# Performance work log

Measured on AMD Instinct MI355X. Metric: run time of the kernel, lower is better.

The kernel has to match this reference:

```python
import jax, jax.numpy as jnp
import numpy as np

EPS = 1e-5   # BatchNorm eps (eval mode, running_mean=0, running_var=1 as at init)
NEG = 0.2    # LeakyReLU negative slope


def _conv(W, x):
    # 1x1 conv == channel matmul. W: [out_c, in_c], x: [B, in_c, ...]
    return jnp.einsum('oc,bc...->bo...', W, x)


def _bn(x, g, b):
    # eval-mode BN with running_mean=0, running_var=1
    sh = (1, -1) + (1,) * (x.ndim - 2)
    return x * (g.reshape(sh) / np.float32(np.sqrt(1.0 + EPS))) + b.reshape(sh)


def _lrelu(x):
    return jax.nn.leaky_relu(x, NEG)


def _knn_idx(pos, k):
    # pos: [B, 3, N] -> idx [B, N, k] of k nearest points (incl. self)
    sq = jnp.sum(pos * pos, axis=1)                      # [B, N]
    inner = jnp.einsum('bcn,bcm->bnm', pos, pos)         # [B, N, N]
    dist = sq[:, :, None] + sq[:, None, :] - 2.0 * inner
    _, idx = jax.lax.top_k(-dist, k)
    return idx


def _gather(points, idx):
    # points [B, N, C], idx [B, N, K] -> [B, N, K, C]
    return jax.vmap(lambda p, i: p[i])(points, idx)


def setup_inputs() -> dict:
    key = jax.random.key(0)
    B, N, K = 2, 8192, 16
    d_points, d_model = 64, 64
    ks = jax.random.split(key, 24)
    w = lambda k_, o, i: (jax.random.normal(k_, (o, i), jnp.float32) * 0.05)
    gm = lambda k_, c: (1.0 + 0.1 * jax.random.normal(k_, (c,), jnp.float32))
    bt = lambda k_, c: (0.1 * jax.random.normal(k_, (c,), jnp.float32))
    return {
        'feats': jax.random.normal(ks[0], (B, d_points, N), jnp.float32),
        'pos': jax.random.uniform(ks[1], (B, 3, N), jnp.float32),
        'k': K,
        'W1': w(ks[2], d_model, d_points), 'g1': gm(ks[3], d_model), 'b1': bt(ks[4], d_model),
        'Wq': w(ks[5], d_model, d_model), 'Wk': w(ks[6], d_model, d_model), 'Wv': w(ks[7], d_model, d_model),
        'Wd1': w(ks[8], d_model, 3), 'gd1': gm(ks[9], d_model), 'bd1': bt(ks[10], d_model),
        'Wd2': w(ks[11], d_model, d_model), 'gd2': gm(ks[12], d_model), 'bd2': bt(ks[13], d_model),
        'Wg1': w(ks[14], d_model, d_model), 'gg1': gm(ks[15], d_model), 'bg1': bt(ks[16], d_model),
        'Wg2': w(ks[17], d_model, d_model), 'gg2': gm(ks[18], d_model), 'bg2': bt(ks[19], d_model),
        'W2': w(ks[20], d_points, d_model), 'g2': gm(ks[21], d_points), 'b2': bt(ks[22], d_points),
    }


def reference(feats, pos, k, W1, g1, b1, Wq, Wk, Wv,
              Wd1, gd1, bd1, Wd2, gd2, bd2,
              Wg1, gg1, bg1, Wg2, gg2, bg2, W2, g2, b2):
    B, _, N = feats.shape
    knn_idx = _knn_idx(pos, k)                            # [B, N, K]
    pos_nc = jnp.transpose(pos, (0, 2, 1))                # [B, N, 3]
    knn_pos = _gather(pos_nc, knn_idx)                    # [B, N, K, 3]

    x = _lrelu(_bn(_conv(W1, feats), g1, b1))             # [B, d, N]
    q = _conv(Wq, x)                                      # [B, d, N]
    k_feat = _gather(jnp.transpose(_conv(Wk, x), (0, 2, 1)), knn_idx)
    k_t = jnp.transpose(k_feat, (0, 3, 2, 1))             # [B, d, K, N]
    v_feat = _gather(jnp.transpose(_conv(Wv, x), (0, 2, 1)), knn_idx)
    v_t = jnp.transpose(v_feat, (0, 3, 2, 1))             # [B, d, K, N]

    rel = pos_nc[:, :, None, :] - knn_pos                 # [B, N, K, 3]
    rel_t = jnp.transpose(rel, (0, 3, 2, 1))              # [B, 3, K, N]
    pe = _lrelu(_bn(_conv(Wd1, rel_t), gd1, bd1))
    pos_enc = _lrelu(_bn(_conv(Wd2, pe), gd2, bd2))       # [B, d, K, N]

    a = q[:, :, None, :] - k_t + pos_enc                  # [B, d, K, N]
    a = _lrelu(_bn(_conv(Wg1, a), gg1, bg1))
    a = _lrelu(_bn(_conv(Wg2, a), gg2, bg2))
    # torch: attn / sqrt(k.size(-1)) where k has shape [B, d, K, N] -> sqrt(N)
    attn = jax.nn.softmax(a / jnp.sqrt(jnp.float32(N)), axis=-2)

    res = jnp.einsum('bmnf,bmnf->bmf', attn, v_t + pos_enc)  # [B, d, N]
    out = _lrelu(_bn(_conv(W2, res), g2, b2)) + feats
    return out
```

## Files before the change

### kernel.cpp

```cpp
#include <hip/hip_runtime.h>
#include <hip/hip_bf16.h>
#include <math.h>

namespace {

constexpr int B = 2;
constexpr int N = 8192;
constexpr int D = 64;
constexpr int GRID = 10;
constexpr int GC = GRID * GRID * GRID;
constexpr float H = 0.1f;
constexpr float NEGS = 0.2f;
constexpr float BN_INV = 0.9999950000374997f;
constexpr float RSQN = 0.011048543456039806f;

typedef __attribute__((ext_vector_type(8))) short bf16x8;
typedef __attribute__((ext_vector_type(16))) float f32x16;

union Frag { int4 i4; unsigned u[4]; bf16x8 h; };

__device__ __forceinline__ float lrelu(float v) { return v > 0.f ? v : NEGS * v; }

__device__ __forceinline__ unsigned pk2(float a, float b) {
  __hip_bfloat162 h2 = __float22bfloat162_rn(make_float2(a, b));
  unsigned r;
  __builtin_memcpy(&r, &h2, 4);
  return r;
}
__device__ __forceinline__ float blo(unsigned u) { return __uint_as_float(u << 16); }
__device__ __forceinline__ float bhi(unsigned u) { return __uint_as_float(u & 0xFFFF0000u); }

__device__ __forceinline__ f32x16 MF(int4 a, const Frag& b, f32x16 c) {
  Frag af; af.i4 = a;
  return __builtin_amdgcn_mfma_f32_32x32x16_bf16(af.h, b.h, c, 0, 0, 0);
}

__device__ __forceinline__ int cellco(float v) {
  int c = (int)(v * 10.0f);
  return min(max(c, 0), GRID - 1);
}

__device__ __forceinline__ void buildB(const f32x16& x0, const f32x16& x1, int h, Frag Bf[4]) {
  unsigned Z[8][2];
  #pragma unroll
  for (int q = 0; q < 4; ++q) {
    Z[q][0]     = pk2(x0[4*q+0], x0[4*q+1]);
    Z[q][1]     = pk2(x0[4*q+2], x0[4*q+3]);
    Z[4+q][0]   = pk2(x1[4*q+0], x1[4*q+1]);
    Z[4+q][1]   = pk2(x1[4*q+2], x1[4*q+3]);
  }
  unsigned S[8][2];
  #pragma unroll
  for (int q = 0; q < 8; ++q) {
    S[q][0] = (unsigned)__shfl_xor((int)Z[q][0], 32);
    S[q][1] = (unsigned)__shfl_xor((int)Z[q][1], 32);
  }
  #pragma unroll
  for (int t = 0; t < 4; ++t) {
    int qq = (t >> 1) * 4 + 2 * (t & 1);
    Bf[t].u[0] = h ? S[qq+1][0] : Z[qq][0];
    Bf[t].u[1] = h ? S[qq+1][1] : Z[qq][1];
    Bf[t].u[2] = h ? Z[qq+1][0] : S[qq][0];
    Bf[t].u[3] = h ? Z[qq+1][1] : S[qq][1];
  }
}

__device__ __forceinline__ f32x16 biasAct(f32x16 d, const float4* bp, int mt, int h) {
  f32x16 r;
  #pragma unroll
  for (int q = 0; q < 4; ++q) {
    float4 bb = bp[h * 8 + mt * 4 + q];
    r[4*q+0] = lrelu(d[4*q+0] + bb.x);
    r[4*q+1] = lrelu(d[4*q+1] + bb.y);
    r[4*q+2] = lrelu(d[4*q+2] + bb.z);
    r[4*q+3] = lrelu(d[4*q+3] + bb.w);
  }
  return r;
}

struct PrepArgs {
  const float* W[9];
  const float* scale[9];
  const float* bias[5];
  const float* bd1;
};

__global__ __launch_bounds__(256) void prep_kernel(PrepArgs a, unsigned short* AF, float* biasAll) {
  int mi = blockIdx.x;
  int tid = threadIdx.x;
  if (mi < 8) {
    int off = (mi == 7) ? 29696 : mi * 4096;
    const float* W = a.W[mi];
    const float* G = a.scale[mi];
    unsigned short* dst = AF + off;
    for (int e = tid; e < 4096; e += 256) {
      int i = e & 7, lane = (e >> 3) & 63, t = (e >> 9) & 3, mt = e >> 11;
      int row = 32 * mt + (lane & 31);
      int k = 16 * t + 8 * (lane >> 5) + i;
      float v = W[row * 64 + k];
      if (G) v *= G[row] * BN_INV;
      __hip_bfloat16 hb = __float2bfloat16(v);
      __builtin_memcpy(&dst[e], &hb, 2);
    }
  } else {
    const float* W = a.W[8];
    const float* G = a.scale[8];
    for (int e = tid; e < 1024; e += 256) {
      int i = e & 7, lane = (e >> 3) & 63, mt = e >> 9;
      int row = 32 * mt + (lane & 31), h = lane >> 5;
      float v = 0.f;
      if (h == 0) {
        if (i < 3) v = W[row * 3 + i] * G[row] * BN_INV;
        else if (i == 3) v = a.bd1[row];
      }
      __hip_bfloat16 hb = __float2bfloat16(v);
      __builtin_memcpy(&AF[28672 + e], &hb, 2);
    }
    for (int e = tid; e < 320; e += 256) {
      int ai = e >> 6, idx = e & 63;
      int h = idx >> 5, mt = (idx >> 4) & 1, q = (idx >> 2) & 3, j = idx & 3;
      biasAll[e] = a.bias[ai][32 * mt + 8 * q + 4 * h + j];
    }
  }
}

__global__ __launch_bounds__(256) void pos4cid_kernel(
    const float* __restrict__ pos, float* __restrict__ pos4,
    int* __restrict__ cid16, int* __restrict__ cellCount)
{
  int i = blockIdx.x * 256 + threadIdx.x;
  int b = i >> 13;
  int n = i & (N - 1);
  const float* pb = pos + (size_t)b * 3 * N;
  float x = pb[n], y = pb[N + n], z = pb[2 * N + n];
  float4 v = {x, y, z, x * x + y * y + z * z};
  *reinterpret_cast<float4*>(pos4 + (size_t)i * 4) = v;
  int cid = (cellco(z) * GRID + cellco(y)) * GRID + cellco(x);
  cid16[i] = cid;
  atomicAdd(&cellCount[b * GC + cid], 1);
}

__global__ __launch_bounds__(1024) void scan_kernel(
    const int* __restrict__ cnt, int* __restrict__ cellStart)
{
  __shared__ int s[2][2048];
  int t = threadIdx.x;
  s[0][t] = cnt[t];
  s[0][t + 1024] = cnt[t + 1024];
  __syncthreads();
  int src = 0;
  for (int off = 1; off < 2048; off <<= 1) {
    int dst = src ^ 1;
    for (int i = t; i < 2048; i += 1024) {
      int v = s[src][i];
      if (i >= off) v += s[src][i - off];
      s[dst][i] = v;
    }
    __syncthreads();
    src ^= 1;
  }
  cellStart[t] = (t == 0) ? 0 : s[src][t - 1];
  cellStart[t + 1024] = s[src][t + 1023];
}

__global__ __launch_bounds__(256) void scatter_kernel(
    const float* __restrict__ pos4, const int* __restrict__ cid16,
    const int* __restrict__ cellStart, int* __restrict__ cellOfs,
    float4* __restrict__ pos4s, int* __restrict__ sid)
{
  int i = blockIdx.x * 256 + threadIdx.x;
  int b = i >> 13;
  int cg = b * GC + cid16[i];
  int dst = cellStart[cg] + atomicAdd(&cellOfs[cg], 1);
  pos4s[dst] = *reinterpret_cast<const float4*>(pos4 + (size_t)i * 4);
  sid[dst] = i & (N - 1);
}

__global__ __launch_bounds__(256) void knn_shell_kernel(
    const float4* __restrict__ pos4s, const int* __restrict__ sid,
    const int* __restrict__ cellStart, int* __restrict__ knn)
{
  constexpr unsigned long long SENT = 0x7F7FFFFFFFFFFFFFULL;
  int lq = threadIdx.x & 15;
  int wid = (blockIdx.x * 256 + threadIdx.x) >> 4;
  int b = wid >> 13;
  float4 q = pos4s[wid];
  int myid = sid[wid];
  int cx = cellco(q.x), cy = cellco(q.y), cz = cellco(q.z);
  const int cbase = b * GC;
  int* orow = knn + ((size_t)b * N + myid) * 16;

  bool done = false;
  #pragma unroll 1
  for (int r = 1; r < GRID; ++r) {
    if (!done) {
      unsigned long long dk[16];
      #pragma unroll
      for (int j = 0; j < 16; ++j) dk[j] = SENT;

      int x0 = max(cx - r, 0), x1 = min(cx + r, GRID - 1);
      int y0 = max(cy - r, 0), y1 = min(cy + r, GRID - 1);
      int z0 = max(cz - r, 0), z1 = min(cz + r, GRID - 1);
      #pragma unroll 1
      for (int zz = z0; zz <= z1; ++zz) {
        #pragma unroll 1
        for (int yy = y0; yy <= y1; ++yy) {
          int rowc = cbase + (zz * GRID + yy) * GRID;
          int i0 = cellStart[rowc + x0], i1 = cellStart[rowc + x1 + 1];
          #pragma unroll 1
          for (int i = i0 + lq; i < i1; i += 16) {
            float4 cp = pos4s[i];
            float inn = q.x * cp.x + q.y * cp.y + q.z * cp.z;
            float dist = fmaxf(fmaf(-2.f, inn, q.w + cp.w), 0.f);
            unsigned long long key =
                ((unsigned long long)__float_as_uint(dist) << 32) | (unsigned)sid[i];
            if (key < dk[15]) {
              bool bj = true;
              #pragma unroll
              for (int j = 15; j >= 1; --j) {
                bool bjm1 = key < dk[j - 1];
                dk[j] = bj ? (bjm1 ? dk[j - 1] : key) : dk[j];
                bj = bjm1;
              }
              if (bj) dk[0] = key;
            }
          }
        }
      }

      float dlast = 0.f;
      #pragma unroll 1
      for (int e = 0; e < 16; ++e) {
        unsigned long long m = dk[0];
        #pragma unroll
        for (int msk = 1; msk <= 8; msk <<= 1) {
          unsigned long long o = __shfl_xor(m, msk);
          m = (o < m) ? o : m;
        }
        if (dk[0] == m) {
          #pragma unroll
          for (int j = 0; j < 15; ++j) dk[j] = dk[j + 1];
          dk[15] = SENT;
        }
        if (lq == 0) orow[e] = (int)(m & 0xFFFFFFFFULL);
        dlast = __uint_as_float((unsigned)(m >> 32));
      }

      float mg = 3.4e38f;
      if (cx - r > 0)        mg = fminf(mg, q.x - (cx - r) * H);
      if (cx + r < GRID - 1) mg = fminf(mg, (cx + r + 1) * H - q.x);
      if (cy - r > 0)        mg = fminf(mg, q.y - (cy - r) * H);
      if (cy + r < GRID - 1) mg = fminf(mg, (cy + r + 1) * H - q.y);
      if (cz - r > 0)        mg = fminf(mg, q.z - (cz - r) * H);
      if (cz + r < GRID - 1) mg = fminf(mg, (cz + r + 1) * H - q.z);
      done = (dlast <= mg * mg * 0.999f);
    }
    if (__all(done)) break;
  }
}

__global__ __launch_bounds__(256) void qkv_kernel(
    const float* __restrict__ feats, const int4* __restrict__ AF,
    const float* __restrict__ b1p,
    uint2* __restrict__ qT, uint2* __restrict__ kT, uint2* __restrict__ vT)
{
  __shared__ int4 sA[2048];
  for (int i = threadIdx.x; i < 2048; i += 256) sA[i] = AF[i];
  __syncthreads();
  int lane = threadIdx.x & 63, w = threadIdx.x >> 6;
  int gw = blockIdx.x * 4 + w;
  int col = lane & 31, h = lane >> 5;
  int nb = gw * 32;
  int b = nb >> 13;
  int n = (nb & (N - 1)) + col;
  size_t gpt = (size_t)b * N + n;
  const float* fb = feats + (size_t)b * D * N + n;

  Frag Bf[4];
  #pragma unroll
  for (int t = 0; t < 4; ++t) {
    int c0 = 16 * t + 8 * h;
    float f[8];
    #pragma unroll
    for (int i = 0; i < 8; ++i) f[i] = fb[(size_t)(c0 + i) * N];
    #pragma unroll
    for (int d_ = 0; d_ < 4; ++d_) Bf[t].u[d_] = pk2(f[2*d_], f[2*d_+1]);
  }
  f32x16 acc0 = {}, acc1 = {};
  #pragma unroll
  for (int t = 0; t < 4; ++t) {
    acc0 = MF(sA[t * 64 + lane], Bf[t], acc0);
    acc1 = MF(sA[(4 + t) * 64 + lane], Bf[t], acc1);
  }
  const float4* bp = (const float4*)b1p;
  f32x16 x0 = biasAct(acc0, bp, 0, h);
  f32x16 x1 = biasAct(acc1, bp, 1, h);
  Frag Bx[4];
  buildB(x0, x1, h, Bx);

  #pragma unroll
  for (int mmat = 0; mmat < 3; ++mmat) {
    const int4* Am = sA + 512 * (mmat + 1);
    uint2* op = (mmat == 0) ? qT : (mmat == 1) ? kT : vT;
    f32x16 a0 = {}, a1 = {};
    #pragma unroll
    for (int t = 0; t < 4; ++t) {
      a0 = MF(Am[t * 64 + lane], Bx[t], a0);
      a1 = MF(Am[(4 + t) * 64 + lane], Bx[t], a1);
    }
    #pragma unroll
    for (int q = 0; q < 4; ++q) {
      uint2 v0, v1;
      v0.x = pk2(a0[4*q+0], a0[4*q+1]); v0.y = pk2(a0[4*q+2], a0[4*q+3]);
      v1.x = pk2(a1[4*q+0], a1[4*q+1]); v1.y = pk2(a1[4*q+2], a1[4*q+3]);
      op[gpt * 16 + 2 * q + h] = v0;
      op[gpt * 16 + 8 + 2 * q + h] = v1;
    }
  }
}

__global__ __launch_bounds__(256) void fused_kernel(
    const float4* __restrict__ pos4, const int* __restrict__ knn,
    const uint2* __restrict__ qT, const uint2* __restrict__ kT, const uint2* __restrict__ vT,
    const int4* __restrict__ AF,
    const float* __restrict__ biases,
    float* __restrict__ res_ws)
{
  __shared__ int4 sA[1664];
  for (int i = threadIdx.x; i < 1664; i += 256) sA[i] = AF[i];
  __syncthreads();
  const float4* bpd2 = (const float4*)(biases);
  const float4* bpg1 = (const float4*)(biases + 64);
  const float4* bpg2 = (const float4*)(biases + 128);

  int lane = threadIdx.x & 63, w = threadIdx.x >> 6;
  int gw = blockIdx.x * 4 + w;
  int col = lane & 31, h = lane >> 5;
  int p = col >> 4, kk = col & 15;
  int pbase = gw * 2;
  int b = pbase >> 13;
  int n = (pbase & (N - 1)) + p;
  size_t g = (size_t)b * N + n;
  int m = knn[g * 16 + kk];
  size_t gm = (size_t)b * N + m;

  float4 P = pos4[g], Q = pos4[gm];
  float rx = P.x - Q.x, ry = P.y - Q.y, rz = P.z - Q.z;

  Frag B0;
  B0.u[0] = h ? 0u : pk2(rx, ry);
  B0.u[1] = h ? 0u : pk2(rz, 1.0f);
  B0.u[2] = 0u; B0.u[3] = 0u;
  f32x16 acc0 = {}, acc1 = {};
  acc0 = MF(sA[1536 + lane], B0, acc0);
  acc1 = MF(sA[1536 + 64 + lane], B0, acc1);
  f32x16 pe0, pe1;
  #pragma unroll
  for (int i = 0; i < 16; ++i) { pe0[i] = lrelu(acc0[i]); pe1[i] = lrelu(acc1[i]); }
  Frag Bp[4];
  buildB(pe0, pe1, h, Bp);

  acc0 = (f32x16){}; acc1 = (f32x16){};
  #pragma unroll
  for (int t = 0; t < 4; ++t) {
    acc0 = MF(sA[t * 64 + lane], Bp[t], acc0);
    acc1 = MF(sA[(4 + t) * 64 + lane], Bp[t], acc1);
  }
  f32x16 pn0 = biasAct(acc0, bpd2, 0, h);
  f32x16 pn1 = biasAct(acc1, bpd2, 1, h);

  unsigned pep[8][2];
  #pragma unroll
  for (int q = 0; q < 4; ++q) {
    pep[q][0]   = pk2(pn0[4*q+0], pn0[4*q+1]);
    pep[q][1]   = pk2(pn0[4*q+2], pn0[4*q+3]);
    pep[4+q][0] = pk2(pn1[4*q+0], pn1[4*q+1]);
    pep[4+q][1] = pk2(pn1[4*q+2], pn1[4*q+3]);
  }

  f32x16 av0, av1;
  #pragma unroll
  for (int mt = 0; mt < 2; ++mt) {
    f32x16& dst = mt ? av1 : av0;
    const f32x16& pn = mt ? pn1 : pn0;
    #pragma unroll
    for (int q = 0; q < 4; ++q) {
      uint2 qv = qT[g * 16 + 8 * mt + 2 * q + h];
      uint2 kv = kT[gm * 16 + 8 * mt + 2 * q + h];
      dst[4*q+0] = pn[4*q+0] + blo(qv.x) - blo(kv.x);
      dst[4*q+1] = pn[4*q+1] + bhi(qv.x) - bhi(kv.x);
      dst[4*q+2] = pn[4*q+2] + blo(qv.y) - blo(kv.y);
      dst[4*q+3] = pn[4*q+3] + bhi(qv.y) - bhi(kv.y);
    }
  }
  buildB(av0, av1, h, Bp);

  acc0 = (f32x16){}; acc1 = (f32x16){};
  #pragma unroll
  for (int t = 0; t < 4; ++t) {
    acc0 = MF(sA[512 + t * 64 + lane], Bp[t], acc0);
    acc1 = MF(sA[512 + (4 + t) * 64 + lane], Bp[t], acc1);
  }
  f32x16 a10 = biasAct(acc0, bpg1, 0, h);
  f32x16 a11 = biasAct(acc1, bpg1, 1, h);
  buildB(a10, a11, h, Bp);

  acc0 = (f32x16){}; acc1 = (f32x16){};
  #pragma unroll
  for (int t = 0; t < 4; ++t) {
    acc0 = MF(sA[1024 + t * 64 + lane], Bp[t], acc0);
    acc1 = MF(sA[1024 + (4 + t) * 64 + lane], Bp[t], acc1);
  }
  f32x16 at0 = biasAct(acc0, bpg2, 0, h);
  f32x16 at1 = biasAct(acc1, bpg2, 1, h);
  #pragma unroll
  for (int i = 0; i < 16; ++i) { at0[i] *= RSQN; at1[i] *= RSQN; }

  float* rp = res_ws + g * 64;
  #pragma unroll
  for (int mt = 0; mt < 2; ++mt) {
    const f32x16& at = mt ? at1 : at0;
    f32x16 ev, nm;
    #pragma unroll
    for (int q = 0; q < 4; ++q) {
      uint2 vv = vT[gm * 16 + 8 * mt + 2 * q + h];
      unsigned pp0 = pep[mt * 4 + q][0], pp1 = pep[mt * 4 + q][1];
      float vp0 = blo(vv.x) + blo(pp0);
      float vp1 = bhi(vv.x) + bhi(pp0);
      float vp2 = blo(vv.y) + blo(pp1);
      float vp3 = bhi(vv.y) + bhi(pp1);
      ev[4*q+0] = __expf(at[4*q+0]); nm[4*q+0] = ev[4*q+0] * vp0;
      ev[4*q+1] = __expf(at[4*q+1]); nm[4*q+1] = ev[4*q+1] * vp1;
      ev[4*q+2] = __expf(at[4*q+2]); nm[4*q+2] = ev[4*q+2] * vp2;
      ev[4*q+3] = __expf(at[4*q+3]); nm[4*q+3] = ev[4*q+3] * vp3;
    }
    #pragma unroll
    for (int i = 0; i < 16; ++i) {
      #pragma unroll
      for (int mask = 1; mask <= 8; mask <<= 1) {
        ev[i] += __shfl_xor(ev[i], mask);
        nm[i] += __shfl_xor(nm[i], mask);
      }
    }
    if (kk == 0) {
      #pragma unroll
      for (int q = 0; q < 4; ++q) {
        float4 r;
        r.x = nm[4*q+0] / ev[4*q+0];
        r.y = nm[4*q+1] / ev[4*q+1];
        r.z = nm[4*q+2] / ev[4*q+2];
        r.w = nm[4*q+3] / ev[4*q+3];
        *(float4*)(rp + 32 * mt + 8 * q + 4 * h) = r;
      }
    }
  }
}

__global__ __launch_bounds__(256) void final_kernel(
    const float* __restrict__ res_ws, const int4* __restrict__ AF,
    const float* __restrict__ b2p, const float* __restrict__ feats,
    float* __restrict__ out)
{
  __shared__ int4 sA[512];
  for (int i = threadIdx.x; i < 512; i += 256) sA[i] = AF[i];
  __syncthreads();
  int lane = threadIdx.x & 63, w = threadIdx.x >> 6;
  int gw = blockIdx.x * 4 + w;
  int col = lane & 31, h = lane >> 5;
  int nb = gw * 32;
  int b = nb >> 13;
  int n = (nb & (N - 1)) + col;
  size_t g = (size_t)b * N + n;
  const float* rp = res_ws + g * 64;
  Frag Br[4];
  #pragma unroll
  for (int t = 0; t < 4; ++t) {
    float4 r0 = *(const float4*)(rp + 16 * t + 8 * h);
    float4 r1 = *(const float4*)(rp + 16 * t + 8 * h + 4);
    Br[t].u[0] = pk2(r0.x, r0.y); Br[t].u[1] = pk2(r0.z, r0.w);
    Br[t].u[2] = pk2(r1.x, r1.y); Br[t].u[3] = pk2(r1.z, r1.w);
  }
  f32x16 a0 = {}, a1 = {};
  #pragma unroll
  for (int t = 0; t < 4; ++t) {
    a0 = MF(sA[t * 64 + lane], Br[t], a0);
    a1 = MF(sA[(4 + t) * 64 + lane], Br[t], a1);
  }
  const float4* bp = (const float4*)b2p;
  f32x16 o0 = biasAct(a0, bp, 0, h);
  f32x16 o1 = biasAct(a1, bp, 1, h);
  const float* fb = feats + (size_t)b * D * N;
  float* ob = out + (size_t)b * D * N;
  #pragma unroll
  for (int mt = 0; mt < 2; ++mt) {
    const f32x16& oo = mt ? o1 : o0;
    #pragma unroll
    for (int q = 0; q < 4; ++q) {
      #pragma unroll
      for (int j = 0; j < 4; ++j) {
        int chan = 32 * mt + 8 * q + 4 * h + j;
        ob[(size_t)chan * N + n] = oo[4*q+j] + fb[(size_t)chan * N + n];
      }
    }
  }
}

}

extern "C" void kernel_launch(void* const* d_in, const int* in_sizes, int n_in,
                              void* d_out, int out_size, void* d_ws, size_t ws_size,
                              hipStream_t stream) {
  const float* feats = (const float*)d_in[0];
  const float* pos   = (const float*)d_in[1];
  const float* W1  = (const float*)d_in[3];
  const float* g1  = (const float*)d_in[4];
  const float* b1  = (const float*)d_in[5];
  const float* Wq  = (const float*)d_in[6];
  const float* Wk  = (const float*)d_in[7];
  const float* Wv  = (const float*)d_in[8];
  const float* Wd1 = (const float*)d_in[9];
  const float* gd1 = (const float*)d_in[10];
  const float* bd1 = (const float*)d_in[11];
  const float* Wd2 = (const float*)d_in[12];
  const float* gd2 = (const float*)d_in[13];
  const float* bd2 = (const float*)d_in[14];
  const float* Wg1 = (const float*)d_in[15];
  const float* gg1 = (const float*)d_in[16];
  const float* bg1 = (const float*)d_in[17];
  const float* Wg2 = (const float*)d_in[18];
  const float* gg2 = (const float*)d_in[19];
  const float* bg2 = (const float*)d_in[20];
  const float* W2  = (const float*)d_in[21];
  const float* g2  = (const float*)d_in[22];
  const float* b2  = (const float*)d_in[23];

  uint8_t* wsb = (uint8_t*)d_ws;
  unsigned short* AF = (unsigned short*)wsb;
  float* biasAll = (float*)(wsb + 73728);
  float* pos4    = (float*)(wsb + 75008);
  uint2* qTb     = (uint2*)(wsb + 337152);
  uint2* kTb     = (uint2*)(wsb + 2434304);
  uint2* vTb     = (uint2*)(wsb + 4531456);
  float* res_ws  = (float*)(wsb + 6628608);
  int*   cid16     = (int*)(wsb + 10822912);
  int*   cellCount = (int*)(wsb + 10888448);
  int*   cellStart = (int*)(wsb + 10896640);
  int*   cellOfs   = (int*)(wsb + 10904832);
  float4* pos4s    = (float4*)(wsb + 10913024);
  int*   sid       = (int*)(wsb + 11175168);
  int*   knn       = (int*)(wsb + 11240704);

  PrepArgs pa;
  pa.W[0] = W1;  pa.W[1] = Wq;  pa.W[2] = Wk;  pa.W[3] = Wv;
  pa.W[4] = Wd2; pa.W[5] = Wg1; pa.W[6] = Wg2; pa.W[7] = W2; pa.W[8] = Wd1;
  pa.scale[0] = g1;  pa.scale[1] = nullptr; pa.scale[2] = nullptr; pa.scale[3] = nullptr;
  pa.scale[4] = gd2; pa.scale[5] = gg1;     pa.scale[6] = gg2;     pa.scale[7] = g2; pa.scale[8] = gd1;
  pa.bias[0] = b1; pa.bias[1] = bd2; pa.bias[2] = bg1; pa.bias[3] = bg2; pa.bias[4] = b2;
  pa.bd1 = bd1;

  hipMemsetAsync(cellCount, 0, 2048 * sizeof(int), stream);
  hipMemsetAsync(cellOfs, 0, 2048 * sizeof(int), stream);
  hipLaunchKernelGGL(prep_kernel, dim3(9), dim3(256), 0, stream, pa, AF, biasAll);
  hipLaunchKernelGGL(pos4cid_kernel, dim3(B * N / 256), dim3(256), 0, stream,
                     pos, pos4, cid16, cellCount);
  hipLaunchKernelGGL(scan_kernel, dim3(1), dim3(1024), 0, stream, cellCount, cellStart);
  hipLaunchKernelGGL(scatter_kernel, dim3(B * N / 256), dim3(256), 0, stream,
                     pos4, cid16, cellStart, cellOfs, pos4s, sid);
  hipLaunchKernelGGL(qkv_kernel, dim3(128), dim3(256), 0, stream,
                     feats, (const int4*)wsb, biasAll, qTb, kTb, vTb);
  hipLaunchKernelGGL(knn_shell_kernel, dim3(B * N / 16), dim3(256), 0, stream,
                     pos4s, sid, cellStart, knn);
  hipLaunchKernelGGL(fused_kernel, dim3(2048), dim3(256), 0, stream,
                     (const float4*)pos4, knn, qTb, kTb, vTb,
                     (const int4*)(wsb + 32768), biasAll + 64, res_ws);
  hipLaunchKernelGGL(final_kernel, dim3(128), dim3(256), 0, stream,
                     res_ws, (const int4*)(wsb + 59392), biasAll + 256, feats, (float*)d_out);
}
```

Before: 151.2 us.

## Fold softmax scale into weights, split qkv grid, bf16 residual, global weight loads

Several changes land at once. The softmax 1/sqrt(N) scale is folded into Wg2 and its bias during prep. qkv_kernel is split across a second grid dimension so each block computes only one of q, k or v, which triples parallelism but recomputes the first conv three times. fused_kernel drops its shared-memory weight staging and reads fragments straight from global memory, and it issues q/k/v gathers earlier to hide latency. The attention result is stored as packed bf16, which halves workspace traffic and lets final_kernel load it directly as fragments, at some precision cost.

```diff
diff --git a/kernel.cpp b/kernel.cpp
--- a/kernel.cpp
+++ b/kernel.cpp
@@ -99,6 +99,7 @@
       int k = 16 * t + 8 * (lane >> 5) + i;
       float v = W[row * 64 + k];
       if (G) v *= G[row] * BN_INV;
+      if (mi == 6) v *= RSQN;
       __hip_bfloat16 hb = __float2bfloat16(v);
       __builtin_memcpy(&dst[e], &hb, 2);
     }
@@ -119,7 +120,9 @@
     for (int e = tid; e < 320; e += 256) {
       int ai = e >> 6, idx = e & 63;
       int h = idx >> 5, mt = (idx >> 4) & 1, q = (idx >> 2) & 3, j = idx & 3;
-      biasAll[e] = a.bias[ai][32 * mt + 8 * q + 4 * h + j];
+      float bv = a.bias[ai][32 * mt + 8 * q + 4 * h + j];
+      if (ai == 3) bv *= RSQN;
+      biasAll[e] = bv;
     }
   }
 }
@@ -264,8 +267,12 @@
     const float* __restrict__ b1p,
     uint2* __restrict__ qT, uint2* __restrict__ kT, uint2* __restrict__ vT)
 {
-  __shared__ int4 sA[2048];
-  for (int i = threadIdx.x; i < 2048; i += 256) sA[i] = AF[i];
+  __shared__ int4 sA[1024];
+  int my = blockIdx.y;
+  for (int i = threadIdx.x; i < 512; i += 256) {
+    sA[i] = AF[i];
+    sA[512 + i] = AF[512 * (1 + my) + i];
+  }
   __syncthreads();
   int lane = threadIdx.x & 63, w = threadIdx.x >> 6;
   int gw = blockIdx.x * 4 + w;
@@ -298,24 +305,20 @@
   Frag Bx[4];
   buildB(x0, x1, h, Bx);
 
-  #pragma unroll
-  for (int mmat = 0; mmat < 3; ++mmat) {
-    const int4* Am = sA + 512 * (mmat + 1);
-    uint2* op = (mmat == 0) ? qT : (mmat == 1) ? kT : vT;
-    f32x16 a0 = {}, a1 = {};
-    #pragma unroll
-    for (int t = 0; t < 4; ++t) {
-      a0 = MF(Am[t * 64 + lane], Bx[t], a0);
-      a1 = MF(Am[(4 + t) * 64 + lane], Bx[t], a1);
-    }
-    #pragma unroll
-    for (int q = 0; q < 4; ++q) {
-      uint2 v0, v1;
-      v0.x = pk2(a0[4*q+0], a0[4*q+1]); v0.y = pk2(a0[4*q+2], a0[4*q+3]);
-      v1.x = pk2(a1[4*q+0], a1[4*q+1]); v1.y = pk2(a1[4*q+2], a1[4*q+3]);
-      op[gpt * 16 + 2 * q + h] = v0;
-      op[gpt * 16 + 8 + 2 * q + h] = v1;
-    }
+  uint2* op = (my == 0) ? qT : (my == 1) ? kT : vT;
+  f32x16 a0 = {}, a1 = {};
+  #pragma unroll
+  for (int t = 0; t < 4; ++t) {
+    a0 = MF(sA[512 + t * 64 + lane], Bx[t], a0);
+    a1 = MF(sA[512 + (4 + t) * 64 + lane], Bx[t], a1);
+  }
+  #pragma unroll
+  for (int q = 0; q < 4; ++q) {
+    uint2 v0, v1;
+    v0.x = pk2(a0[4*q+0], a0[4*q+1]); v0.y = pk2(a0[4*q+2], a0[4*q+3]);
+    v1.x = pk2(a1[4*q+0], a1[4*q+1]); v1.y = pk2(a1[4*q+2], a1[4*q+3]);
+    op[gpt * 16 + 2 * q + h] = v0;
+    op[gpt * 16 + 8 + 2 * q + h] = v1;
   }
 }
 
@@ -324,11 +327,8 @@
     const uint2* __restrict__ qT, const uint2* __restrict__ kT, const uint2* __restrict__ vT,
     const int4* __restrict__ AF,
     const float* __restrict__ biases,
-    float* __restrict__ res_ws)
-{
-  __shared__ int4 sA[1664];
-  for (int i = threadIdx.x; i < 1664; i += 256) sA[i] = AF[i];
-  __syncthreads();
+    uint2* __restrict__ res_ws)
+{
   const float4* bpd2 = (const float4*)(biases);
   const float4* bpg1 = (const float4*)(biases + 64);
   const float4* bpg2 = (const float4*)(biases + 128);
@@ -345,6 +345,14 @@
   size_t gm = (size_t)b * N + m;
 
   float4 P = pos4[g], Q = pos4[gm];
+
+  uint2 qv[8], kv[8];
+  #pragma unroll
+  for (int i = 0; i < 8; ++i) {
+    qv[i] = qT[g * 16 + 2 * i + h];
+    kv[i] = kT[gm * 16 + 2 * i + h];
+  }
+
   float rx = P.x - Q.x, ry = P.y - Q.y, rz = P.z - Q.z;
 
   Frag B0;
@@ -352,8 +360,8 @@
   B0.u[1] = h ? 0u : pk2(rz, 1.0f);
   B0.u[2] = 0u; B0.u[3] = 0u;
   f32x16 acc0 = {}, acc1 = {};
-  acc0 = MF(sA[1536 + lane], B0, acc0);
-  acc1 = MF(sA[1536 + 64 + lane], B0, acc1);
+  acc0 = MF(AF[1536 + lane], B0, acc0);
+  acc1 = MF(AF[1600 + lane], B0, acc1);
   f32x16 pe0, pe1;
   #pragma unroll
   for (int i = 0; i < 16; ++i) { pe0[i] = lrelu(acc0[i]); pe1[i] = lrelu(acc1[i]); }
@@ -363,8 +371,8 @@
   acc0 = (f32x16){}; acc1 = (f32x16){};
   #pragma unroll
   for (int t = 0; t < 4; ++t) {
-    acc0 = MF(sA[t * 64 + lane], Bp[t], acc0);
-    acc1 = MF(sA[(4 + t) * 64 + lane], Bp[t], acc1);
+    acc0 = MF(AF[t * 64 + lane], Bp[t], acc0);
+    acc1 = MF(AF[(4 + t) * 64 + lane], Bp[t], acc1);
   }
   f32x16 pn0 = biasAct(acc0, bpd2, 0, h);
   f32x16 pn1 = biasAct(acc1, bpd2, 1, h);
@@ -385,21 +393,25 @@
     const f32x16& pn = mt ? pn1 : pn0;
     #pragma unroll
     for (int q = 0; q < 4; ++q) {
-      uint2 qv = qT[g * 16 + 8 * mt + 2 * q + h];
-      uint2 kv = kT[gm * 16 + 8 * mt + 2 * q + h];
-      dst[4*q+0] = pn[4*q+0] + blo(qv.x) - blo(kv.x);
-      dst[4*q+1] = pn[4*q+1] + bhi(qv.x) - bhi(kv.x);
-      dst[4*q+2] = pn[4*q+2] + blo(qv.y) - blo(kv.y);
-      dst[4*q+3] = pn[4*q+3] + bhi(qv.y) - bhi(kv.y);
+      uint2 qq_ = qv[4 * mt + q];
+      uint2 kq_ = kv[4 * mt + q];
+      dst[4*q+0] = pn[4*q+0] + blo(qq_.x) - blo(kq_.x);
+      dst[4*q+1] = pn[4*q+1] + bhi(qq_.x) - bhi(kq_.x);
+      dst[4*q+2] = pn[4*q+2] + blo(qq_.y) - blo(kq_.y);
+      dst[4*q+3] = pn[4*q+3] + bhi(qq_.y) - bhi(kq_.y);
     }
   }
   buildB(av0, av1, h, Bp);
 
+  uint2 vv[8];
+  #pragma unroll
+  for (int i = 0; i < 8; ++i) vv[i] = vT[gm * 16 + 2 * i + h];
+
   acc0 = (f32x16){}; acc1 = (f32x16){};
   #pragma unroll
   for (int t = 0; t < 4; ++t) {
-    acc0 = MF(sA[512 + t * 64 + lane], Bp[t], acc0);
-    acc1 = MF(sA[512 + (4 + t) * 64 + lane], Bp[t], acc1);
+    acc0 = MF(AF[512 + t * 64 + lane], Bp[t], acc0);
+    acc1 = MF(AF[512 + (4 + t) * 64 + lane], Bp[t], acc1);
   }
   f32x16 a10 = biasAct(acc0, bpg1, 0, h);
   f32x16 a11 = biasAct(acc1, bpg1, 1, h);
@@ -408,27 +420,24 @@
   acc0 = (f32x16){}; acc1 = (f32x16){};
   #pragma unroll
   for (int t = 0; t < 4; ++t) {
-    acc0 = MF(sA[1024 + t * 64 + lane], Bp[t], acc0);
-    acc1 = MF(sA[1024 + (4 + t) * 64 + lane], Bp[t], acc1);
+    acc0 = MF(AF[1024 + t * 64 + lane], Bp[t], acc0);
+    acc1 = MF(AF[1024 + (4 + t) * 64 + lane], Bp[t], acc1);
   }
   f32x16 at0 = biasAct(acc0, bpg2, 0, h);
   f32x16 at1 = biasAct(acc1, bpg2, 1, h);
-  #pragma unroll
-  for (int i = 0; i < 16; ++i) { at0[i] *= RSQN; at1[i] *= RSQN; }
-
-  float* rp = res_ws + g * 64;
+
   #pragma unroll
   for (int mt = 0; mt < 2; ++mt) {
     const f32x16& at = mt ? at1 : at0;
     f32x16 ev, nm;
     #pragma unroll
     for (int q = 0; q < 4; ++q) {
-      uint2 vv = vT[gm * 16 + 8 * mt + 2 * q + h];
+      uint2 vq_ = vv[4 * mt + q];
       unsigned pp0 = pep[mt * 4 + q][0], pp1 = pep[mt * 4 + q][1];
-      float vp0 = blo(vv.x) + blo(pp0);
-      float vp1 = bhi(vv.x) + bhi(pp0);
-      float vp2 = blo(vv.y) + blo(pp1);
-      float vp3 = bhi(vv.y) + bhi(pp1);
+      float vp0 = blo(vq_.x) + blo(pp0);
+      float vp1 = bhi(vq_.x) + bhi(pp0);
+      float vp2 = blo(vq_.y) + blo(pp1);
+      float vp3 = bhi(vq_.y) + bhi(pp1);
       ev[4*q+0] = __expf(at[4*q+0]); nm[4*q+0] = ev[4*q+0] * vp0;
       ev[4*q+1] = __expf(at[4*q+1]); nm[4*q+1] = ev[4*q+1] * vp1;
       ev[4*q+2] = __expf(at[4*q+2]); nm[4*q+2] = ev[4*q+2] * vp2;
@@ -445,19 +454,17 @@
     if (kk == 0) {
       #pragma unroll
       for (int q = 0; q < 4; ++q) {
-        float4 r;
-        r.x = nm[4*q+0] / ev[4*q+0];
-        r.y = nm[4*q+1] / ev[4*q+1];
-        r.z = nm[4*q+2] / ev[4*q+2];
-        r.w = nm[4*q+3] / ev[4*q+3];
-        *(float4*)(rp + 32 * mt + 8 * q + 4 * h) = r;
+        uint2 rr;
+        rr.x = pk2(nm[4*q+0] / ev[4*q+0], nm[4*q+1] / ev[4*q+1]);
+        rr.y = pk2(nm[4*q+2] / ev[4*q+2], nm[4*q+3] / ev[4*q+3]);
+        res_ws[g * 16 + 8 * mt + 2 * q + h] = rr;
       }
     }
   }
 }
 
 __global__ __launch_bounds__(256) void final_kernel(
-    const float* __restrict__ res_ws, const int4* __restrict__ AF,
+    const uint2* __restrict__ res_ws, const int4* __restrict__ AF,
     const float* __restrict__ b2p, const float* __restrict__ feats,
     float* __restrict__ out)
 {
@@ -471,15 +478,10 @@
   int b = nb >> 13;
   int n = (nb & (N - 1)) + col;
   size_t g = (size_t)b * N + n;
-  const float* rp = res_ws + g * 64;
+  const int4* rp = (const int4*)(res_ws + (size_t)g * 16);
   Frag Br[4];
   #pragma unroll
-  for (int t = 0; t < 4; ++t) {
-    float4 r0 = *(const float4*)(rp + 16 * t + 8 * h);
-    float4 r1 = *(const float4*)(rp + 16 * t + 8 * h + 4);
-    Br[t].u[0] = pk2(r0.x, r0.y); Br[t].u[1] = pk2(r0.z, r0.w);
-    Br[t].u[2] = pk2(r1.x, r1.y); Br[t].u[3] = pk2(r1.z, r1.w);
-  }
+  for (int t = 0; t < 4; ++t) Br[t].i4 = rp[2 * t + h];
   f32x16 a0 = {}, a1 = {};
   #pragma unroll
   for (int t = 0; t < 4; ++t) {
@@ -541,7 +543,7 @@
   uint2* qTb     = (uint2*)(wsb + 337152);
   uint2* kTb     = (uint2*)(wsb + 2434304);
   uint2* vTb     = (uint2*)(wsb + 4531456);
-  float* res_ws  = (float*)(wsb + 6628608);
+  uint2* res_ws  = (uint2*)(wsb + 6628608);
   int*   cid16     = (int*)(wsb + 10822912);
   int*   cellCount = (int*)(wsb + 10888448);
   int*   cellStart = (int*)(wsb + 10896640);
@@ -566,7 +568,7 @@
   hipLaunchKernelGGL(scan_kernel, dim3(1), dim3(1024), 0, stream, cellCount, cellStart);
   hipLaunchKernelGGL(scatter_kernel, dim3(B * N / 256), dim3(256), 0, stream,
                      pos4, cid16, cellStart, cellOfs, pos4s, sid);
-  hipLaunchKernelGGL(qkv_kernel, dim3(128), dim3(256), 0, stream,
+  hipLaunchKernelGGL(qkv_kernel, dim3(128, 3), dim3(256), 0, stream,
                      feats, (const int4*)wsb, biasAll, qTb, kTb, vTb);
   hipLaunchKernelGGL(knn_shell_kernel, dim3(B * N / 16), dim3(256), 0, stream,
                      pos4s, sid, cellStart, knn);
```

Result: slower. 154.6 us (+2.3%).
